# Kernel optimization log

Measured on AMD Instinct MI355X. Metric: run time of the kernel, lower is better.

## Reference

```python
import jax, jax.numpy as jnp
import numpy as np

M, K, N, GROUP = 32, 8192, 28672, 128


def setup_inputs() -> dict:
    key = jax.random.key(0)
    k1, k2, k3, k4 = jax.random.split(key, 4)
    x = jax.random.normal(k1, (M, K), dtype=jnp.float16)
    # int32 words, each packing 8 consecutive int4 values along K
    qweight = jax.random.randint(k2, (K // 8, N), 0, 2147483647, dtype=jnp.int32)
    scales = (jax.random.uniform(k3, (K // GROUP, N), dtype=jnp.float32) * 0.01 + 0.001).astype(jnp.float16)
    bias = (jax.random.normal(k4, (N,), dtype=jnp.float32) * 0.02).astype(jnp.float16)
    return {"x": x, "qweight": qweight, "scales": scales, "bias": bias}


def reference(x, qweight, scales, bias):
    # Unpack 8 int4 nibbles per int32 word along K: (K//8, N) -> (K, N)
    K8, n = qweight.shape
    shifts = (jnp.arange(8, dtype=jnp.int32) * 4)[None, :, None]
    wq = ((qweight[:, None, :] >> shifts) & 15).reshape(K8 * 8, n)  # [K, N] in [0,15]
    # Dequant: zero-point fixed at 8 (pack() asserts zeros==8), per-group scales
    w = wq.astype(jnp.float16) - jnp.float16(8.0)
    g, gs = scales.shape[0], (K8 * 8) // scales.shape[0]
    w = (w.reshape(g, gs, n) * scales[:, None, :]).reshape(K8 * 8, n)  # [K, N] fp16
    return jnp.dot(x, w) + bias  # [M, N]
```

## Files before the change

kernel.cpp:

```cpp
#include <hip/hip_runtime.h>
#include <stdint.h>

#define K_DIM 8192
#define N_DIM 28672

typedef _Float16 half8 __attribute__((ext_vector_type(8)));
typedef _Float16 half2t __attribute__((ext_vector_type(2)));
typedef float f32x16 __attribute__((ext_vector_type(16)));

__global__ __launch_bounds__(256) void prep_x(const float* __restrict__ x,
                                              _Float16* __restrict__ xp) {
  int idx = blockIdx.x * 256 + threadIdx.x;
  int m  = idx & 31;
  int k8 = idx >> 5;
  const float* p = x + (size_t)m * K_DIM + (size_t)k8 * 8;
  float4 xa = *(const float4*)p;
  float4 xb = *(const float4*)(p + 4);
  half2t p0 = __builtin_bit_cast(half2t, __builtin_amdgcn_cvt_pkrtz(xa.x, xb.x));
  half2t p1 = __builtin_bit_cast(half2t, __builtin_amdgcn_cvt_pkrtz(xa.y, xb.y));
  half2t p2 = __builtin_bit_cast(half2t, __builtin_amdgcn_cvt_pkrtz(xa.z, xb.z));
  half2t p3 = __builtin_bit_cast(half2t, __builtin_amdgcn_cvt_pkrtz(xa.w, xb.w));
  half8 o;
  o[0] = p0[0]; o[1] = p0[1]; o[2] = p1[0]; o[3] = p1[1];
  o[4] = p2[0]; o[5] = p2[1]; o[6] = p3[0]; o[7] = p3[1];
  *(half8*)(xp + ((size_t)k8 * 32 + m) * 8) = o;
}

static __device__ __forceinline__ half8 dqs(uint32_t w, half2t sh) {
  const uint32_t M4 = 0x000F000Fu, E = 0x64006400u;
  half2t off; off[0] = (_Float16)(-1032.0f); off[1] = (_Float16)(-1032.0f);
  half2t v0 = (__builtin_bit_cast(half2t, ( w        & M4) | E) + off) * sh;
  half2t v1 = (__builtin_bit_cast(half2t, ((w >> 4)  & M4) | E) + off) * sh;
  half2t v2 = (__builtin_bit_cast(half2t, ((w >> 8)  & M4) | E) + off) * sh;
  half2t v3 = (__builtin_bit_cast(half2t, ((w >> 12) & M4) | E) + off) * sh;
  half8 r;
  r[0] = v0[0]; r[1] = v0[1]; r[2] = v1[0]; r[3] = v1[1];
  r[4] = v2[0]; r[5] = v2[1]; r[6] = v3[0]; r[7] = v3[1];
  return r;
}

__global__ __launch_bounds__(256, 4) void qgemm(
    const uint32_t* __restrict__ q, const float* __restrict__ scales,
    const float* __restrict__ bias, const _Float16* __restrict__ xp,
    float* __restrict__ out) {
  __shared__ float red[4][32][32];
  const int tid  = threadIdx.x;
  const int w    = tid >> 6;
  const int lane = tid & 63;
  const int h    = lane >> 5;
  const int nl   = lane & 31;
  const int col0 = blockIdx.x << 5;
  const int wr0  = w << 8;

  const uint32_t* qp = q + (size_t)(wr0 + h) * N_DIM + col0 + nl;
  const half8*    ap = (const half8*)xp + (size_t)(wr0 + h) * 32 + nl;
  const float*    sp = scales + (size_t)(w << 4) * N_DIM + col0 + nl;

  uint32_t qb[3][8];
  half8    ab[2][8];
  float    sb[2];

  auto loadQ = [&](int g, uint32_t (&dst)[8]) {
#pragma unroll
    for (int i = 0; i < 8; i++)
      dst[i] = qp[(size_t)(16 * g + 2 * i) * N_DIM];
  };
  auto loadA = [&](int g, half8 (&dst)[8]) {
#pragma unroll
    for (int i = 0; i < 8; i++)
      dst[i] = ap[(size_t)(16 * g + 2 * i) * 32];
  };

  f32x16 acc;
#pragma unroll
  for (int j = 0; j < 16; j++) acc[j] = 0.0f;

  loadQ(0, qb[0]);
  loadA(0, ab[0]);
  sb[0] = sp[0];
  loadQ(1, qb[1]);

#pragma unroll
  for (int g = 0; g < 16; g++) {
    if (g + 1 < 16) {
      loadA(g + 1, ab[(g + 1) & 1]);
      sb[(g + 1) & 1] = sp[(size_t)(g + 1) * N_DIM];
    }
    if (g + 2 < 16) loadQ(g + 2, qb[(g + 2) % 3]);
    float s = sb[g & 1];
    half2t sh = __builtin_bit_cast(half2t, __builtin_amdgcn_cvt_pkrtz(s, s));
#pragma unroll
    for (int i = 0; i < 8; i++)
      acc = __builtin_amdgcn_mfma_f32_32x32x16_f16(
          ab[g & 1][i], dqs(qb[g % 3][i], sh), acc, 0, 0, 0);
  }

#pragma unroll
  for (int j = 0; j < 16; j++) {
    int row = (j & 3) + ((j >> 2) << 3) + (h << 2);
    red[w][row][nl] = acc[j];
  }
  __syncthreads();

  const int col = tid & 31;
  const int r0  = tid >> 5;
  float bz = bias[col0 + col];
#pragma unroll
  for (int i = 0; i < 4; i++) {
    int row = r0 + (i << 3);
    float v = red[0][row][col] + red[1][row][col] +
              red[2][row][col] + red[3][row][col];
    out[(size_t)row * N_DIM + col0 + col] = v + bz;
  }
}

extern "C" void kernel_launch(void* const* d_in, const int* in_sizes, int n_in,
                              void* d_out, int out_size, void* d_ws, size_t ws_size,
                              hipStream_t stream) {
  const float*    xf      = (const float*)d_in[0];
  const uint32_t* qweight = (const uint32_t*)d_in[1];
  const float*    scales  = (const float*)d_in[2];
  const float*    bias    = (const float*)d_in[3];
  float*          out     = (float*)d_out;
  _Float16*       xp      = (_Float16*)d_ws;

  prep_x<<<dim3(128), dim3(256), 0, stream>>>(xf, xp);
  qgemm<<<dim3(N_DIM / 32), dim3(256), 0, stream>>>(qweight, scales, bias, xp, out);
}
```

Baseline: 209.8 us.

## Widen split-K to sixteen waves per block and drop manual prefetch pipeline

Each block now runs 1024 threads, so sixteen waves each reduce a 512-deep K slice instead of four waves over 2048. The explicit triple/double-buffered register prefetch is replaced by direct loads inside an unrolled loop, and the final reduction sums sixteen partials in shared memory. The aim is more waves in flight to hide global memory latency on this bandwidth-bound int4 GEMV-like workload. In exchange the shared reduction buffer grows to 64KB per block, which limits blocks per CU, and the code relies on the compiler to schedule loads ahead.

```diff
diff --git a/kernel.cpp b/kernel.cpp
--- a/kernel.cpp
+++ b/kernel.cpp
@@ -39,60 +39,41 @@
   return r;
 }
 
-__global__ __launch_bounds__(256, 4) void qgemm(
+__global__ __launch_bounds__(1024, 8) void qgemm(
     const uint32_t* __restrict__ q, const float* __restrict__ scales,
     const float* __restrict__ bias, const _Float16* __restrict__ xp,
     float* __restrict__ out) {
-  __shared__ float red[4][32][32];
+  __shared__ float red[16][32][32];
   const int tid  = threadIdx.x;
   const int w    = tid >> 6;
   const int lane = tid & 63;
   const int h    = lane >> 5;
   const int nl   = lane & 31;
   const int col0 = blockIdx.x << 5;
-  const int wr0  = w << 8;
+  const int wr0  = w << 6;
 
   const uint32_t* qp = q + (size_t)(wr0 + h) * N_DIM + col0 + nl;
   const half8*    ap = (const half8*)xp + (size_t)(wr0 + h) * 32 + nl;
-  const float*    sp = scales + (size_t)(w << 4) * N_DIM + col0 + nl;
+  const float*    sp = scales + (size_t)(w << 2) * N_DIM + col0 + nl;
 
-  uint32_t qb[3][8];
-  half8    ab[2][8];
-  float    sb[2];
-
-  auto loadQ = [&](int g, uint32_t (&dst)[8]) {
+  float s4[4];
 #pragma unroll
-    for (int i = 0; i < 8; i++)
-      dst[i] = qp[(size_t)(16 * g + 2 * i) * N_DIM];
-  };
-  auto loadA = [&](int g, half8 (&dst)[8]) {
-#pragma unroll
-    for (int i = 0; i < 8; i++)
-      dst[i] = ap[(size_t)(16 * g + 2 * i) * 32];
-  };
+  for (int g = 0; g < 4; g++) s4[g] = sp[(size_t)g * N_DIM];
 
   f32x16 acc;
 #pragma unroll
   for (int j = 0; j < 16; j++) acc[j] = 0.0f;
 
-  loadQ(0, qb[0]);
-  loadA(0, ab[0]);
-  sb[0] = sp[0];
-  loadQ(1, qb[1]);
-
 #pragma unroll
-  for (int g = 0; g < 16; g++) {
-    if (g + 1 < 16) {
-      loadA(g + 1, ab[(g + 1) & 1]);
-      sb[(g + 1) & 1] = sp[(size_t)(g + 1) * N_DIM];
+  for (int g = 0; g < 4; g++) {
+    half2t sh = __builtin_bit_cast(half2t, __builtin_amdgcn_cvt_pkrtz(s4[g], s4[g]));
+#pragma unroll
+    for (int i = 0; i < 8; i++) {
+      int r = 16 * g + 2 * i;
+      half8 af = ap[(size_t)r * 32];
+      acc = __builtin_amdgcn_mfma_f32_32x32x16_f16(af, dqs(qp[(size_t)r * N_DIM], sh),
+                                                   acc, 0, 0, 0);
     }
-    if (g + 2 < 16) loadQ(g + 2, qb[(g + 2) % 3]);
-    float s = sb[g & 1];
-    half2t sh = __builtin_bit_cast(half2t, __builtin_amdgcn_cvt_pkrtz(s, s));
-#pragma unroll
-    for (int i = 0; i < 8; i++)
-      acc = __builtin_amdgcn_mfma_f32_32x32x16_f16(
-          ab[g & 1][i], dqs(qb[g % 3][i], sh), acc, 0, 0, 0);
   }
 
 #pragma unroll
@@ -102,16 +83,12 @@
   }
   __syncthreads();
 
+  const int row = tid >> 5;
   const int col = tid & 31;
-  const int r0  = tid >> 5;
-  float bz = bias[col0 + col];
+  float v = bias[col0 + col];
 #pragma unroll
-  for (int i = 0; i < 4; i++) {
-    int row = r0 + (i << 3);
-    float v = red[0][row][col] + red[1][row][col] +
-              red[2][row][col] + red[3][row][col];
-    out[(size_t)row * N_DIM + col0 + col] = v + bz;
-  }
+  for (int i = 0; i < 16; i++) v += red[i][row][col];
+  out[(size_t)row * N_DIM + col0 + col] = v;
 }
 
 extern "C" void kernel_launch(void* const* d_in, const int* in_sizes, int n_in,
@@ -125,5 +102,5 @@
   _Float16*       xp      = (_Float16*)d_ws;
 
   prep_x<<<dim3(128), dim3(256), 0, stream>>>(xf, xp);
-  qgemm<<<dim3(N_DIM / 32), dim3(256), 0, stream>>>(qweight, scales, bias, xp, out);
+  qgemm<<<dim3(N_DIM / 32), dim3(1024), 0, stream>>>(qweight, scales, bias, xp, out);
 }
```

After: 208.9 us. No clear change (-0.4%).
